# Kernel tuning notes

Measured on AMD Instinct MI355X. Metric: run time of the kernel, lower is better.

The kernel has to match this reference:

```python
import jax, jax.numpy as jnp
import numpy as np

B, T, N, D = 16, 12, 1024, 128
M, TOPK = 64, 16


def _ln(x, eps=1e-5):
    mu = x.mean(-1, keepdims=True)
    var = ((x - mu) ** 2).mean(-1, keepdims=True)
    return (x - mu) / jnp.sqrt(var + eps)


def setup_inputs() -> dict:
    key = jax.random.key(0)
    ks = jax.random.split(key, 18)
    s = 1.0 / np.sqrt(D)
    inp = {
        "x": jax.random.normal(ks[0], (B, T, N, D), jnp.float32),
        "eigvec": jax.random.normal(ks[1], (D, N, 1), jnp.float32),
        "eigvalue": jax.random.normal(ks[2], (D,), jnp.float32),
        "Wq": jax.random.normal(ks[3], (D, D), jnp.float32) * s,
        "bq": jax.random.normal(ks[4], (D,), jnp.float32) * 0.01,
        "Wk": jax.random.normal(ks[5], (D, D), jnp.float32) * s,
        "bk": jax.random.normal(ks[6], (D,), jnp.float32) * 0.01,
        "Wv": jax.random.normal(ks[7], (D, D), jnp.float32) * s,
        "bv": jax.random.normal(ks[8], (D,), jnp.float32) * 0.01,
        "Wo": jax.random.normal(ks[9], (D, D), jnp.float32) * s,
        "bo": jax.random.normal(ks[10], (D,), jnp.float32) * 0.01,
        "node_emb": jax.random.normal(ks[11], (M, 2 * D), jnp.float32),
        "ffW1": jax.random.normal(ks[12], (D, D), jnp.float32) * s,
        "ffb1": jax.random.normal(ks[13], (D,), jnp.float32) * 0.01,
        "ffW2": jax.random.normal(ks[14], (D, D), jnp.float32) * s,
        "ffb2": jax.random.normal(ks[15], (D,), jnp.float32) * 0.01,
        "adj": jax.random.randint(ks[16], (N, 16), 0, N),
    }
    return inp


def reference(x, eigvec, eigvalue, Wq, bq, Wk, bk, Wv, bv, Wo, bo,
              node_emb, ffW1, ffb1, ffW2, ffb2, adj):
    # spectral positional term: [N,D] = eigvec^T scaled per-column by eigvalue
    x_ = x + eigvec[:, :, 0].T * eigvalue  # [B,T,N,D]

    Q = x_ @ Wq + bq
    K = x_ @ Wk + bk
    V = x_ @ Wv + bv

    # node selection: memory embeddings attend over concat(Q,K) features
    nodevec3 = jnp.concatenate([Q, K], axis=-1)  # [B,T,N,2D]
    supports2 = jax.nn.softmax(jnp.einsum('me,btne->btmn', node_emb, nodevec3), axis=-1)
    _, idx = jax.lax.top_k(supports2, TOPK)  # idx: [B,T,M,TOPK]
    idx_flat = idx.reshape(B, T, M * TOPK)

    def gather(t):  # t: [B,T,N,D] -> [B,T,M,TOPK,D]
        return jnp.take_along_axis(t, idx_flat[..., None], axis=2).reshape(B, T, M, TOPK, D)

    selQ, selK, selV = gather(Q), gather(K), gather(V)

    attn = jax.nn.softmax(
        jnp.einsum('btmkd,btmjd->btmkj', selQ, selK) / np.sqrt(D), axis=-1)
    node_new = jnp.einsum('btmkj,btmjd->btmkd', attn, selV).reshape(B, T, M * TOPK, D)

    # scatter_add aggregation back to the N nodes, normalized by hit counts
    b_ix = jnp.arange(B)[:, None, None]
    t_ix = jnp.arange(T)[None, :, None]
    dict1 = jnp.zeros((B, T, N, D), x.dtype).at[b_ix, t_ix, idx_flat].add(node_new)
    counts = jnp.full((B, T, N), 1e-14, x.dtype).at[b_ix, t_ix, idx_flat].add(1.0)
    value = dict1 / counts[..., None]

    value = (value @ Wo + bo) + x_
    value = _ln(value)
    h = jax.nn.relu(value @ ffW1 + ffb1) @ ffW2 + ffb2
    return _ln(h + value)
```

## Files before the change

### kernel.cpp

```cpp
#include <hip/hip_runtime.h>
#include <math.h>

#define RTOT   196608
#define NNODE  1024
#define NBT    192

typedef __attribute__((ext_vector_type(8))) short short8;
typedef __attribute__((ext_vector_type(4))) float f32x4;

__device__ __forceinline__ unsigned short f2bf(float f) {
  unsigned u = __float_as_uint(f);
  return (unsigned short)((u + 0x7fffu + ((u >> 16) & 1u)) >> 16);
}
__device__ __forceinline__ float bf2f(unsigned short b) {
  return __uint_as_float(((unsigned)b) << 16);
}

__global__ __launch_bounds__(256) void pos_kernel(
    const float* __restrict__ eigvec, const float* __restrict__ eigval,
    float* __restrict__ pos) {
  int i = blockIdx.x * 256 + threadIdx.x;
  int d = i >> 10, n = i & 1023;
  pos[n * 128 + d] = eigvec[d * 1024 + n] * eigval[d];
}

__global__ __launch_bounds__(256) void prepw_kernel(
    const float* __restrict__ W0, const float* __restrict__ W1,
    const float* __restrict__ W2, const float* __restrict__ W3,
    const float* __restrict__ W4, const float* __restrict__ W5,
    unsigned short* __restrict__ out) {
  int i = blockIdx.x * 256 + threadIdx.x;
  int wsel = i >> 14, rem = i & 16383, c = rem >> 7, k = rem & 127;
  const float* W = (wsel == 0) ? W0 : (wsel == 1) ? W1 : (wsel == 2) ? W2
                 : (wsel == 3) ? W3 : (wsel == 4) ? W4 : W5;
  out[i] = f2bf(W[k * 128 + c]);
}

__global__ __launch_bounds__(256) void wcomb_kernel(
    const float* __restrict__ Wq, const float* __restrict__ Wk,
    const float* __restrict__ bq, const float* __restrict__ bk,
    const float* __restrict__ emb, float* __restrict__ Wcomb,
    float* __restrict__ bcomb) {
  int i = blockIdx.x * 256 + threadIdx.x;
  if (i < 8192) {
    int k = i >> 6, m = i & 63;
    float s = 0.f;
    for (int d = 0; d < 128; ++d)
      s += Wq[k * 128 + d] * emb[m * 256 + d]
         + Wk[k * 128 + d] * emb[m * 256 + 128 + d];
    Wcomb[i] = s;
  } else if (i < 8256) {
    int m = i - 8192;
    float s = 0.f;
    for (int d = 0; d < 128; ++d)
      s += bq[d] * emb[m * 256 + d] + bk[d] * emb[m * 256 + 128 + d];
    bcomb[m] = s;
  }
}

template<int NCOL, int KCHUNKS, int ADDPOS, int HASBIAS, int WRITEXB>
__global__ __launch_bounds__(256, 2) void gemm_k(
    const float* __restrict__ A1, const float* __restrict__ A2,
    const float* __restrict__ W, const float* __restrict__ bias,
    const float* __restrict__ pos, unsigned short* __restrict__ xb,
    float* __restrict__ out) {
  __shared__ float As[128 * 64];
  __shared__ float Ws[64 * NCOL];
  constexpr int JW = (NCOL == 128) ? 2 : 1;
  const int tid = threadIdx.x;
  const int tx = tid & 15, ty = tid >> 4;
  const int row0 = blockIdx.x * 128;

  float acc[8][4 * JW];
#pragma unroll
  for (int i = 0; i < 8; ++i)
#pragma unroll
    for (int j = 0; j < 4 * JW; ++j) acc[i][j] = 0.f;

  for (int kc = 0; kc < KCHUNKS; ++kc) {
    const int kt = kc * 64;
    const float* __restrict__ Asrc = (kt < 128) ? A1 : A2;
    const int kbase = kt & 127;
#pragma unroll
    for (int i = 0; i < 8; ++i) {
      int f = tid + 256 * i;
      int m = f >> 4;
      int k4 = (f & 15) << 2;
      int r = row0 + m;
      float4 a = *(const float4*)&Asrc[(size_t)r * 128 + kbase + k4];
      if constexpr (ADDPOS) {
        float4 p = *(const float4*)&pos[(r & 1023) * 128 + kbase + k4];
        a.x += p.x; a.y += p.y; a.z += p.z; a.w += p.w;
      }
      if constexpr (WRITEXB) {
        unsigned lo = (unsigned)f2bf(a.x) | ((unsigned)f2bf(a.y) << 16);
        unsigned hi = (unsigned)f2bf(a.z) | ((unsigned)f2bf(a.w) << 16);
        *(uint2*)&xb[(size_t)r * 128 + kbase + k4] = make_uint2(lo, hi);
      }
      *(float4*)&As[m * 64 + k4] = a;
    }
#pragma unroll
    for (int i = 0; i < NCOL / 16; ++i) {
      int f = tid + 256 * i;
      int kk = f / (NCOL / 4);
      int c4 = (f % (NCOL / 4)) << 2;
      *(float4*)&Ws[kk * NCOL + c4] =
          *(const float4*)&W[(size_t)(kt + kk) * NCOL + c4];
    }
    __syncthreads();
    for (int k4 = 0; k4 < 64; k4 += 4) {
      float a[8][4];
#pragma unroll
      for (int i = 0; i < 8; ++i)
        *(float4*)&a[i][0] = *(const float4*)&As[(ty * 8 + i) * 64 + k4];
#pragma unroll
      for (int kk = 0; kk < 4; ++kk) {
        float4 w0 = *(const float4*)&Ws[(k4 + kk) * NCOL + tx * 4];
        float4 w1;
        if constexpr (JW == 2)
          w1 = *(const float4*)&Ws[(k4 + kk) * NCOL + 64 + tx * 4];
#pragma unroll
        for (int i = 0; i < 8; ++i) {
          float av = a[i][kk];
          acc[i][0] = fmaf(av, w0.x, acc[i][0]);
          acc[i][1] = fmaf(av, w0.y, acc[i][1]);
          acc[i][2] = fmaf(av, w0.z, acc[i][2]);
          acc[i][3] = fmaf(av, w0.w, acc[i][3]);
          if constexpr (JW == 2) {
            acc[i][4] = fmaf(av, w1.x, acc[i][4]);
            acc[i][5] = fmaf(av, w1.y, acc[i][5]);
            acc[i][6] = fmaf(av, w1.z, acc[i][6]);
            acc[i][7] = fmaf(av, w1.w, acc[i][7]);
          }
        }
      }
    }
    __syncthreads();
  }
  float4 b0 = make_float4(0.f, 0.f, 0.f, 0.f);
  float4 b1 = make_float4(0.f, 0.f, 0.f, 0.f);
  if constexpr (HASBIAS) {
    b0 = *(const float4*)&bias[tx * 4];
    if constexpr (JW == 2) b1 = *(const float4*)&bias[64 + tx * 4];
  }
#pragma unroll
  for (int i = 0; i < 8; ++i) {
    const int r = row0 + ty * 8 + i;
    {
      float4 o = make_float4(acc[i][0] + b0.x, acc[i][1] + b0.y,
                             acc[i][2] + b0.z, acc[i][3] + b0.w);
      *(float4*)&out[(size_t)r * NCOL + tx * 4] = o;
    }
    if constexpr (JW == 2) {
      float4 o = make_float4(acc[i][4] + b1.x, acc[i][5] + b1.y,
                             acc[i][6] + b1.z, acc[i][7] + b1.w);
      *(float4*)&out[(size_t)r * NCOL + 64 + tx * 4] = o;
    }
  }
}

template<int EPI>
__global__ __launch_bounds__(256, 2) void gemm_mfma(
    const unsigned short* __restrict__ A, const unsigned short* __restrict__ Bt,
    const float* __restrict__ bias, const float* __restrict__ x,
    const float* __restrict__ pos, const unsigned short* __restrict__ resb,
    float* __restrict__ outf, unsigned short* __restrict__ outb) {
  __shared__ float lds_s[128][2];
  __shared__ float lds_q[128][2];
  const int tid = threadIdx.x;
  const int w = tid >> 6, lane = tid & 63;
  const int wr = w >> 1, wc = w & 1;
  const int lhi = lane >> 4, llo = lane & 15;
  const int r0 = blockIdx.x * 128;

  short8 bf[4][4];
#pragma unroll
  for (int j = 0; j < 4; ++j)
#pragma unroll
    for (int kq = 0; kq < 4; ++kq)
      bf[j][kq] = *(const short8*)&Bt[(size_t)(wc * 64 + j * 16 + llo) * 128 +
                                      kq * 32 + lhi * 8];
  f32x4 acc[4][4];
#pragma unroll
  for (int i = 0; i < 4; ++i)
#pragma unroll
    for (int j = 0; j < 4; ++j) acc[i][j] = (f32x4)(0.0f);

#pragma unroll
  for (int i = 0; i < 4; ++i) {
    short8 af[4];
#pragma unroll
    for (int kq = 0; kq < 4; ++kq)
      af[kq] = *(const short8*)&A[(size_t)(r0 + wr * 64 + i * 16 + llo) * 128 +
                                  kq * 32 + lhi * 8];
#pragma unroll
    for (int kq = 0; kq < 4; ++kq)
#pragma unroll
      for (int j = 0; j < 4; ++j)
        acc[i][j] = __builtin_amdgcn_mfma_f32_16x16x32_bf16(
            af[kq], bf[j][kq], acc[i][j], 0, 0, 0);
  }

  float bvals[4];
#pragma unroll
  for (int j = 0; j < 4; ++j) bvals[j] = bias[wc * 64 + j * 16 + llo];

  if constexpr (EPI == 1 || EPI == 3) {
#pragma unroll
    for (int i = 0; i < 4; ++i) {
#pragma unroll
      for (int reg = 0; reg < 4; ++reg) {
        const int rl = wr * 64 + i * 16 + lhi * 4 + reg;
        const int r = r0 + rl;
        float s = 0.f, q = 0.f;
#pragma unroll
        for (int j = 0; j < 4; ++j) {
          const int c = wc * 64 + j * 16 + llo;
          float vv = acc[i][j][reg] + bvals[j];
          if constexpr (EPI == 1)
            vv += x[(size_t)r * 128 + c] + pos[(r & 1023) * 128 + c];
          else
            vv += bf2f(resb[(size_t)r * 128 + c]);
          acc[i][j][reg] = vv;
          s += vv; q += vv * vv;
        }
#pragma unroll
        for (int m = 1; m < 16; m <<= 1) {
          s += __shfl_xor(s, m);
          q += __shfl_xor(q, m);
        }
        if (llo == 0) { lds_s[rl][wc] = s; lds_q[rl][wc] = q; }
      }
    }
    __syncthreads();
#pragma unroll
    for (int i = 0; i < 4; ++i) {
#pragma unroll
      for (int reg = 0; reg < 4; ++reg) {
        const int rl = wr * 64 + i * 16 + lhi * 4 + reg;
        const int r = r0 + rl;
        float s = lds_s[rl][0] + lds_s[rl][1];
        float q = lds_q[rl][0] + lds_q[rl][1];
        float mu = s * (1.f / 128.f);
        float rstd = rsqrtf(q * (1.f / 128.f) - mu * mu + 1e-5f);
#pragma unroll
        for (int j = 0; j < 4; ++j) {
          const int c = wc * 64 + j * 16 + llo;
          float vv = (acc[i][j][reg] - mu) * rstd;
          if constexpr (EPI == 1)
            outb[(size_t)r * 128 + c] = f2bf(vv);
          else
            outf[(size_t)r * 128 + c] = vv;
        }
      }
    }
  } else {
#pragma unroll
    for (int i = 0; i < 4; ++i)
#pragma unroll
      for (int reg = 0; reg < 4; ++reg) {
        const int rl = wr * 64 + i * 16 + lhi * 4 + reg;
        const int r = r0 + rl;
#pragma unroll
        for (int j = 0; j < 4; ++j) {
          const int c = wc * 64 + j * 16 + llo;
          float vv = acc[i][j][reg] + bvals[j];
          if constexpr (EPI == 2) {
            vv = fmaxf(vv, 0.f);
            outb[(size_t)r * 128 + c] = f2bf(vv);
          } else {
            outf[(size_t)r * 128 + c] = vv;
          }
        }
      }
  }
}

__global__ __launch_bounds__(256) void topk_kernel(
    const float* __restrict__ S, int* __restrict__ idx_out) {
  __shared__ float sc[8 * 1024];
  const int tid = threadIdx.x;
  const int bt = blockIdx.x >> 3, mg = blockIdx.x & 7;
#pragma unroll
  for (int u = 0; u < 8; ++u) {
    int f = tid + 256 * u;
    int n = f >> 1, half = f & 1;
    float4 v = *(const float4*)&S[((size_t)bt * 1024 + n) * 64 + mg * 8 + half * 4];
    sc[(half * 4 + 0) * 1024 + n] = v.x;
    sc[(half * 4 + 1) * 1024 + n] = v.y;
    sc[(half * 4 + 2) * 1024 + n] = v.z;
    sc[(half * 4 + 3) * 1024 + n] = v.w;
  }
  __syncthreads();
  const int lane = tid & 63, w = tid >> 6;
  for (int ml = w * 2; ml < w * 2 + 2; ++ml) {
    float v[16];
#pragma unroll
    for (int q = 0; q < 4; ++q) {
      float4 t = *(const float4*)&sc[ml * 1024 + lane * 16 + q * 4];
      v[q * 4 + 0] = t.x; v[q * 4 + 1] = t.y;
      v[q * 4 + 2] = t.z; v[q * 4 + 3] = t.w;
    }
    const int outbase = (bt * 64 + mg * 8 + ml) << 4;
    for (int it = 0; it < 16; ++it) {
      float mv = v[0]; int li = 0;
#pragma unroll
      for (int u = 1; u < 16; ++u) {
        if (v[u] > mv) { mv = v[u]; li = u; }
      }
      int mi = (lane << 4) + li;
#pragma unroll
      for (int off = 1; off < 64; off <<= 1) {
        float ov = __shfl_xor(mv, off);
        int oi = __shfl_xor(mi, off);
        if (ov > mv || (ov == mv && oi < mi)) { mv = ov; mi = oi; }
      }
      bool mine = (mi >> 4) == lane;
      int rm = mi & 15;
#pragma unroll
      for (int u = 0; u < 16; ++u)
        if (mine && rm == u) v[u] = -3.402823466e38f;
      if (lane == 0) idx_out[outbase + it] = mi;
    }
  }
}

__global__ __launch_bounds__(256) void attn_dense(
    const float* __restrict__ Q, const float* __restrict__ K,
    const float* __restrict__ V, const int* __restrict__ idx,
    unsigned short* __restrict__ node_new) {
  __shared__ float sQ[16 * 132], sK[16 * 132], sV[16 * 132];
  __shared__ float sP[16 * 16];
  __shared__ int sidx[16];
  const int tid = threadIdx.x;
  const int bt = blockIdx.x >> 6, m = blockIdx.x & 63;
  if (tid < 16) sidx[tid] = idx[((bt * 64 + m) << 4) + tid];
  __syncthreads();
  const size_t base = (size_t)bt * 1024 * 128;
#pragma unroll
  for (int u = 0; u < 6; ++u) {
    int f = tid + 256 * u;
    int mat = f >> 9;
    int r = (f >> 5) & 15;
    int c4 = (f & 31) << 2;
    const float* src = (mat == 0) ? Q : (mat == 1) ? K : V;
    float* dst = (mat == 0) ? sQ : (mat == 1) ? sK : sV;
    *(float4*)&dst[r * 132 + c4] =
        *(const float4*)&src[base + (size_t)sidx[r] * 128 + c4];
  }
  __syncthreads();
  const int kk = tid >> 4, jj = tid & 15;
  float s = 0.f;
#pragma unroll
  for (int c4 = 0; c4 < 128; c4 += 4) {
    float4 q = *(const float4*)&sQ[kk * 132 + c4];
    float4 kv = *(const float4*)&sK[jj * 132 + c4];
    s = fmaf(q.x, kv.x, s); s = fmaf(q.y, kv.y, s);
    s = fmaf(q.z, kv.z, s); s = fmaf(q.w, kv.w, s);
  }
  s *= 0.08838834764831845f;
  float mx = s;
#pragma unroll
  for (int off = 8; off >= 1; off >>= 1) mx = fmaxf(mx, __shfl_xor(mx, off, 16));
  float e = expf(s - mx);
  float sum = e;
#pragma unroll
  for (int off = 8; off >= 1; off >>= 1) sum += __shfl_xor(sum, off, 16);
  sP[kk * 16 + jj] = e / sum;
  __syncthreads();
  const int dc = tid & 15;
  const int d0 = dc * 8;
  float o[8] = {0.f, 0.f, 0.f, 0.f, 0.f, 0.f, 0.f, 0.f};
#pragma unroll
  for (int j = 0; j < 16; ++j) {
    float p = sP[kk * 16 + j];
    float4 v0 = *(const float4*)&sV[j * 132 + d0];
    float4 v1 = *(const float4*)&sV[j * 132 + d0 + 4];
    o[0] = fmaf(p, v0.x, o[0]); o[1] = fmaf(p, v0.y, o[1]);
    o[2] = fmaf(p, v0.z, o[2]); o[3] = fmaf(p, v0.w, o[3]);
    o[4] = fmaf(p, v1.x, o[4]); o[5] = fmaf(p, v1.y, o[5]);
    o[6] = fmaf(p, v1.z, o[6]); o[7] = fmaf(p, v1.w, o[7]);
  }
  unsigned short* orow = node_new + base + (size_t)(m * 16 + kk) * 128 + d0;
  uint4 st;
  st.x = (unsigned)f2bf(o[0]) | ((unsigned)f2bf(o[1]) << 16);
  st.y = (unsigned)f2bf(o[2]) | ((unsigned)f2bf(o[3]) << 16);
  st.z = (unsigned)f2bf(o[4]) | ((unsigned)f2bf(o[5]) << 16);
  st.w = (unsigned)f2bf(o[6]) | ((unsigned)f2bf(o[7]) << 16);
  *(uint4*)orow = st;
}

__global__ __launch_bounds__(256) void build_lists(
    const int* __restrict__ idx, int* __restrict__ lists,
    int* __restrict__ counts) {
  int i = blockIdx.x * 256 + threadIdx.x;
  int bt = i >> 10, j = i & 1023;
  int n = idx[i];
  int slot = atomicAdd(&counts[bt * 1024 + n], 1);
  lists[(size_t)(bt * 1024 + n) * 64 + slot] = j;
}

__global__ __launch_bounds__(256) void gather_sum(
    const unsigned short* __restrict__ node_new, const int* __restrict__ lists,
    const int* __restrict__ counts, unsigned short* __restrict__ outb) {
  const int lane = threadIdx.x & 63;
  const int row = blockIdx.x * 4 + (threadIdx.x >> 6);
  const int cnt = counts[row];
  const int bt = row >> 10;
  const float inv = 1.0f / ((float)cnt + 1e-14f);
  const int* lp = lists + (size_t)row * 64;
  float ax = 0.f, ay = 0.f;
  for (int j = 0; j < cnt; ++j) {
    int src = lp[j];
    unsigned u = *(const unsigned*)&node_new[((size_t)bt * 1024 + src) * 128 + lane * 2];
    ax += bf2f(u & 0xffff); ay += bf2f(u >> 16);
  }
  ax *= inv; ay *= inv;
  unsigned pk = (unsigned)f2bf(ax) | ((unsigned)f2bf(ay) << 16);
  *(unsigned*)&outb[(size_t)row * 128 + lane * 2] = pk;
}

extern "C" void kernel_launch(void* const* d_in, const int* in_sizes, int n_in,
                              void* d_out, int out_size, void* d_ws, size_t ws_size,
                              hipStream_t stream) {
  const float* x      = (const float*)d_in[0];
  const float* eigvec = (const float*)d_in[1];
  const float* eigval = (const float*)d_in[2];
  const float* Wq     = (const float*)d_in[3];
  const float* bq     = (const float*)d_in[4];
  const float* Wk     = (const float*)d_in[5];
  const float* bk     = (const float*)d_in[6];
  const float* Wv     = (const float*)d_in[7];
  const float* bv     = (const float*)d_in[8];
  const float* Wo     = (const float*)d_in[9];
  const float* bo     = (const float*)d_in[10];
  const float* nemb   = (const float*)d_in[11];
  const float* ffW1   = (const float*)d_in[12];
  const float* ffb1   = (const float*)d_in[13];
  const float* ffW2   = (const float*)d_in[14];
  const float* ffb2   = (const float*)d_in[15];
  float* outp = (float*)d_out;

  char* ws = (char*)d_ws;
  float*          pos    = (float*)(ws + 0);
  int*            idxp   = (int*)  (ws + 524288);
  int*            counts = (int*)  (ws + 1310720);
  float*          Wcomb  = (float*)(ws + 1310720);
  float*          bcomb  = (float*)(ws + 1343488);
  unsigned short* Wtall  = (unsigned short*)(ws + 2097152);
  unsigned short* xb     = (unsigned short*)(ws + 2293760);
  float*          R1     = (float*)(ws + 52625408);
  float*          R2     = (float*)(ws + 153288704);
  float*          Sbuf   = (float*)(ws + 253952000);
  unsigned short* Wt_q = Wtall;
  unsigned short* Wt_k = Wtall + 16384;
  unsigned short* Wt_v = Wtall + 32768;
  unsigned short* Wt_o = Wtall + 49152;
  unsigned short* Wt_1 = Wtall + 65536;
  unsigned short* Wt_2 = Wtall + 81920;
  unsigned short* vln  = xb;
  unsigned short* h1   = (unsigned short*)R1;
  int*            lists = (int*)R2;
  unsigned short* nnb  = (unsigned short*)Sbuf;
  float*          Qbuf = outp;
  unsigned short* dictb = (unsigned short*)d_out;

  pos_kernel<<<512, 256, 0, stream>>>(eigvec, eigval, pos);
  prepw_kernel<<<384, 256, 0, stream>>>(Wq, Wk, Wv, Wo, ffW1, ffW2, Wtall);
  wcomb_kernel<<<33, 256, 0, stream>>>(Wq, Wk, bq, bk, nemb, Wcomb, bcomb);

  gemm_k<64, 2, 1, 1, 1><<<1536, 256, 0, stream>>>(
      x, nullptr, Wcomb, bcomb, pos, xb, Sbuf);
  topk_kernel<<<1536, 256, 0, stream>>>(Sbuf, idxp);

  gemm_mfma<0><<<1536, 256, 0, stream>>>(
      xb, Wt_q, bq, nullptr, nullptr, nullptr, Qbuf, nullptr);
  gemm_mfma<0><<<1536, 256, 0, stream>>>(
      xb, Wt_k, bk, nullptr, nullptr, nullptr, R1, nullptr);
  gemm_mfma<0><<<1536, 256, 0, stream>>>(
      xb, Wt_v, bv, nullptr, nullptr, nullptr, R2, nullptr);

  attn_dense<<<12288, 256, 0, stream>>>(Qbuf, R1, R2, idxp, nnb);

  hipMemsetAsync(counts, 0, (size_t)NBT * NNODE * 4, stream);
  build_lists<<<768, 256, 0, stream>>>(idxp, lists, counts);
  gather_sum<<<49152, 256, 0, stream>>>(nnb, lists, counts, dictb);

  gemm_mfma<1><<<1536, 256, 0, stream>>>(
      dictb, Wt_o, bo, x, pos, nullptr, nullptr, vln);
  gemm_mfma<2><<<1536, 256, 0, stream>>>(
      vln, Wt_1, ffb1, nullptr, nullptr, nullptr, nullptr, h1);
  gemm_mfma<3><<<1536, 256, 0, stream>>>(
      h1, Wt_2, ffb2, nullptr, nullptr, vln, outp, nullptr);
}
```

Measured before the change: 690.8 us.

## Fuse Q/K/V GEMMs into one bf16-output kernel and use bitonic-threshold top-k

Replaces three separate fp32-output Q, K and V GEMM launches with one kernel that loads the A tile once, loops over the three weight matrices and writes bf16 outputs. attn_dense now reads those bf16 tensors and converts them to fp32 in LDS. The top-k selection changes from 16 serial argmax/shuffle rounds to a per-lane bitonic sort, a cross-lane merge to find the 16th-largest value, and a threshold pass that emits indices through an LDS atomic counter. LDS rows are padded to avoid bank conflicts. The new top-k emits indices in arbitrary order and handles ties differently, and the bf16 Q/K/V lose some precision.

```diff
diff --git a/kernel.cpp b/kernel.cpp
--- a/kernel.cpp
+++ b/kernel.cpp
@@ -159,6 +159,69 @@
   }
 }
 
+__global__ __launch_bounds__(256, 2) void gemm_qkv(
+    const unsigned short* __restrict__ A, const unsigned short* __restrict__ Wt,
+    const float* __restrict__ bq, const float* __restrict__ bk,
+    const float* __restrict__ bv,
+    unsigned short* __restrict__ outq, unsigned short* __restrict__ outk,
+    unsigned short* __restrict__ outv) {
+  const int tid = threadIdx.x;
+  const int w = tid >> 6, lane = tid & 63;
+  const int wr = w >> 1, wc = w & 1;
+  const int lhi = lane >> 4, llo = lane & 15;
+  const int r0 = blockIdx.x * 128;
+
+  short8 af[4][4];
+#pragma unroll
+  for (int i = 0; i < 4; ++i)
+#pragma unroll
+    for (int kq = 0; kq < 4; ++kq)
+      af[i][kq] = *(const short8*)&A[(size_t)(r0 + wr * 64 + i * 16 + llo) * 128 +
+                                     kq * 32 + lhi * 8];
+#pragma unroll
+  for (int s = 0; s < 3; ++s) {
+    const unsigned short* __restrict__ Bt = Wt + s * 16384;
+    const float* __restrict__ bias = (s == 0) ? bq : (s == 1) ? bk : bv;
+    unsigned short* __restrict__ outb = (s == 0) ? outq : (s == 1) ? outk : outv;
+
+    short8 bf[4][4];
+#pragma unroll
+    for (int j = 0; j < 4; ++j)
+#pragma unroll
+      for (int kq = 0; kq < 4; ++kq)
+        bf[j][kq] = *(const short8*)&Bt[(size_t)(wc * 64 + j * 16 + llo) * 128 +
+                                        kq * 32 + lhi * 8];
+    f32x4 acc[4][4];
+#pragma unroll
+    for (int i = 0; i < 4; ++i)
+#pragma unroll
+      for (int j = 0; j < 4; ++j) acc[i][j] = (f32x4)(0.0f);
+#pragma unroll
+    for (int i = 0; i < 4; ++i)
+#pragma unroll
+      for (int kq = 0; kq < 4; ++kq)
+#pragma unroll
+        for (int j = 0; j < 4; ++j)
+          acc[i][j] = __builtin_amdgcn_mfma_f32_16x16x32_bf16(
+              af[i][kq], bf[j][kq], acc[i][j], 0, 0, 0);
+
+    float bvals[4];
+#pragma unroll
+    for (int j = 0; j < 4; ++j) bvals[j] = bias[wc * 64 + j * 16 + llo];
+#pragma unroll
+    for (int i = 0; i < 4; ++i)
+#pragma unroll
+      for (int reg = 0; reg < 4; ++reg) {
+        const int r = r0 + wr * 64 + i * 16 + lhi * 4 + reg;
+#pragma unroll
+        for (int j = 0; j < 4; ++j) {
+          const int c = wc * 64 + j * 16 + llo;
+          outb[(size_t)r * 128 + c] = f2bf(acc[i][j][reg] + bvals[j]);
+        }
+      }
+  }
+}
+
 template<int EPI>
 __global__ __launch_bounds__(256, 2) void gemm_mfma(
     const unsigned short* __restrict__ A, const unsigned short* __restrict__ Bt,
@@ -278,56 +341,85 @@
 
 __global__ __launch_bounds__(256) void topk_kernel(
     const float* __restrict__ S, int* __restrict__ idx_out) {
-  __shared__ float sc[8 * 1024];
+  __shared__ float sc[8 * 1088];
+  __shared__ int cnt[8];
   const int tid = threadIdx.x;
   const int bt = blockIdx.x >> 3, mg = blockIdx.x & 7;
+  if (tid < 8) cnt[tid] = 0;
 #pragma unroll
   for (int u = 0; u < 8; ++u) {
     int f = tid + 256 * u;
     int n = f >> 1, half = f & 1;
     float4 v = *(const float4*)&S[((size_t)bt * 1024 + n) * 64 + mg * 8 + half * 4];
-    sc[(half * 4 + 0) * 1024 + n] = v.x;
-    sc[(half * 4 + 1) * 1024 + n] = v.y;
-    sc[(half * 4 + 2) * 1024 + n] = v.z;
-    sc[(half * 4 + 3) * 1024 + n] = v.w;
+    int p = (n >> 4) * 17 + (n & 15);
+    sc[(half * 4 + 0) * 1088 + p] = v.x;
+    sc[(half * 4 + 1) * 1088 + p] = v.y;
+    sc[(half * 4 + 2) * 1088 + p] = v.z;
+    sc[(half * 4 + 3) * 1088 + p] = v.w;
   }
   __syncthreads();
   const int lane = tid & 63, w = tid >> 6;
-  for (int ml = w * 2; ml < w * 2 + 2; ++ml) {
-    float v[16];
-#pragma unroll
-    for (int q = 0; q < 4; ++q) {
-      float4 t = *(const float4*)&sc[ml * 1024 + lane * 16 + q * 4];
-      v[q * 4 + 0] = t.x; v[q * 4 + 1] = t.y;
-      v[q * 4 + 2] = t.z; v[q * 4 + 3] = t.w;
-    }
+  for (int h2 = 0; h2 < 2; ++h2) {
+    const int ml = w * 2 + h2;
+    float ov[16], r[16];
+#pragma unroll
+    for (int j = 0; j < 16; ++j) {
+      float t = sc[ml * 1088 + lane * 17 + j];
+      ov[j] = t; r[j] = t;
+    }
+#pragma unroll
+    for (int k = 2; k <= 16; k <<= 1) {
+#pragma unroll
+      for (int d = k >> 1; d >= 1; d >>= 1) {
+#pragma unroll
+        for (int i = 0; i < 16; ++i) {
+          int j = i ^ d;
+          if (j > i) {
+            bool up = ((i & k) == 0);
+            float a = r[i], b = r[j];
+            float mn = fminf(a, b), mx = fmaxf(a, b);
+            r[i] = up ? mn : mx;
+            r[j] = up ? mx : mn;
+          }
+        }
+      }
+    }
+#pragma unroll
+    for (int md = 1; md < 64; md <<= 1) {
+      float c[16];
+#pragma unroll
+      for (int i = 0; i < 16; ++i)
+        c[i] = fmaxf(r[i], __shfl_xor(r[15 - i], md));
+#pragma unroll
+      for (int d = 8; d >= 1; d >>= 1) {
+#pragma unroll
+        for (int i = 0; i < 16; ++i) {
+          int j = i ^ d;
+          if (j > i) {
+            float a = c[i], b = c[j];
+            c[i] = fminf(a, b);
+            c[j] = fmaxf(a, b);
+          }
+        }
+      }
+#pragma unroll
+      for (int i = 0; i < 16; ++i) r[i] = c[i];
+    }
+    const float tstar = r[0];
     const int outbase = (bt * 64 + mg * 8 + ml) << 4;
-    for (int it = 0; it < 16; ++it) {
-      float mv = v[0]; int li = 0;
-#pragma unroll
-      for (int u = 1; u < 16; ++u) {
-        if (v[u] > mv) { mv = v[u]; li = u; }
-      }
-      int mi = (lane << 4) + li;
-#pragma unroll
-      for (int off = 1; off < 64; off <<= 1) {
-        float ov = __shfl_xor(mv, off);
-        int oi = __shfl_xor(mi, off);
-        if (ov > mv || (ov == mv && oi < mi)) { mv = ov; mi = oi; }
-      }
-      bool mine = (mi >> 4) == lane;
-      int rm = mi & 15;
-#pragma unroll
-      for (int u = 0; u < 16; ++u)
-        if (mine && rm == u) v[u] = -3.402823466e38f;
-      if (lane == 0) idx_out[outbase + it] = mi;
+#pragma unroll
+    for (int j = 0; j < 16; ++j) {
+      if (ov[j] >= tstar) {
+        int s = atomicAdd(&cnt[ml], 1);
+        if (s < 16) idx_out[outbase + s] = lane * 16 + j;
+      }
     }
   }
 }
 
 __global__ __launch_bounds__(256) void attn_dense(
-    const float* __restrict__ Q, const float* __restrict__ K,
-    const float* __restrict__ V, const int* __restrict__ idx,
+    const unsigned short* __restrict__ Q, const unsigned short* __restrict__ K,
+    const unsigned short* __restrict__ V, const int* __restrict__ idx,
     unsigned short* __restrict__ node_new) {
   __shared__ float sQ[16 * 132], sK[16 * 132], sV[16 * 132];
   __shared__ float sP[16 * 16];
@@ -338,15 +430,21 @@
   __syncthreads();
   const size_t base = (size_t)bt * 1024 * 128;
 #pragma unroll
-  for (int u = 0; u < 6; ++u) {
+  for (int u = 0; u < 3; ++u) {
     int f = tid + 256 * u;
-    int mat = f >> 9;
-    int r = (f >> 5) & 15;
-    int c4 = (f & 31) << 2;
-    const float* src = (mat == 0) ? Q : (mat == 1) ? K : V;
+    int mat = f >> 8;
+    int rem = f & 255;
+    int r = rem >> 4;
+    int c8 = (rem & 15) << 3;
+    const unsigned short* src = (mat == 0) ? Q : (mat == 1) ? K : V;
     float* dst = (mat == 0) ? sQ : (mat == 1) ? sK : sV;
-    *(float4*)&dst[r * 132 + c4] =
-        *(const float4*)&src[base + (size_t)sidx[r] * 128 + c4];
+    uint4 raw = *(const uint4*)&src[base + (size_t)sidx[r] * 128 + c8];
+    float4 f0 = make_float4(bf2f(raw.x & 0xffff), bf2f(raw.x >> 16),
+                            bf2f(raw.y & 0xffff), bf2f(raw.y >> 16));
+    float4 f1 = make_float4(bf2f(raw.z & 0xffff), bf2f(raw.z >> 16),
+                            bf2f(raw.w & 0xffff), bf2f(raw.w >> 16));
+    *(float4*)&dst[r * 132 + c8] = f0;
+    *(float4*)&dst[r * 132 + c8 + 4] = f1;
   }
   __syncthreads();
   const int kk = tid >> 4, jj = tid & 15;
@@ -449,20 +547,17 @@
   float*          bcomb  = (float*)(ws + 1343488);
   unsigned short* Wtall  = (unsigned short*)(ws + 2097152);
   unsigned short* xb     = (unsigned short*)(ws + 2293760);
-  float*          R1     = (float*)(ws + 52625408);
-  float*          R2     = (float*)(ws + 153288704);
-  float*          Sbuf   = (float*)(ws + 253952000);
-  unsigned short* Wt_q = Wtall;
-  unsigned short* Wt_k = Wtall + 16384;
-  unsigned short* Wt_v = Wtall + 32768;
+  unsigned short* Kb     = (unsigned short*)(ws + 52625408);
+  unsigned short* Vb     = (unsigned short*)(ws + 102957056);
+  float*          Sbuf   = (float*)(ws + 153288704);
   unsigned short* Wt_o = Wtall + 49152;
   unsigned short* Wt_1 = Wtall + 65536;
   unsigned short* Wt_2 = Wtall + 81920;
   unsigned short* vln  = xb;
-  unsigned short* h1   = (unsigned short*)R1;
-  int*            lists = (int*)R2;
+  unsigned short* h1   = Kb;
+  int*            lists = (int*)Vb;
   unsigned short* nnb  = (unsigned short*)Sbuf;
-  float*          Qbuf = outp;
+  unsigned short* Qb   = (unsigned short*)d_out;
   unsigned short* dictb = (unsigned short*)d_out;
 
   pos_kernel<<<512, 256, 0, stream>>>(eigvec, eigval, pos);
@@ -473,14 +568,9 @@
       x, nullptr, Wcomb, bcomb, pos, xb, Sbuf);
   topk_kernel<<<1536, 256, 0, stream>>>(Sbuf, idxp);
 
-  gemm_mfma<0><<<1536, 256, 0, stream>>>(
-      xb, Wt_q, bq, nullptr, nullptr, nullptr, Qbuf, nullptr);
-  gemm_mfma<0><<<1536, 256, 0, stream>>>(
-      xb, Wt_k, bk, nullptr, nullptr, nullptr, R1, nullptr);
-  gemm_mfma<0><<<1536, 256, 0, stream>>>(
-      xb, Wt_v, bv, nullptr, nullptr, nullptr, R2, nullptr);
-
-  attn_dense<<<12288, 256, 0, stream>>>(Qbuf, R1, R2, idxp, nnb);
+  gemm_qkv<<<1536, 256, 0, stream>>>(xb, Wtall, bq, bk, bv, Qb, Kb, Vb);
+
+  attn_dense<<<12288, 256, 0, stream>>>(Qb, Kb, Vb, idxp, nnb);
 
   hipMemsetAsync(counts, 0, (size_t)NBT * NNODE * 4, stream);
   build_lists<<<768, 256, 0, stream>>>(idxp, lists, counts);
```

After: 600.4 us. 1.15x faster.
